# Kernel optimization log

Hardware: AMD Instinct MI355X
Metric: run time of the kernel (lower is better)

The kernel has to match this reference:

```python
import jax, jax.numpy as jnp
import numpy as np

ALPHA = 0.01  # ema_decay

def setup_inputs() -> dict:
    key = jax.random.key(0)
    k1, k2 = jax.random.split(key)
    B, S, H = 8, 2048, 2048
    x = jax.random.normal(k1, (B, S, H), dtype=jnp.float32)
    W = jax.random.normal(k2, (H, H), dtype=jnp.float32) * (1.0 / np.sqrt(H))
    b = jnp.zeros((H,), dtype=jnp.float32)
    return {"x": x, "W": W, "b": b}

def reference(x, W, b):
    B, S, H = x.shape
    dt = x.dtype
    # p = [S-1, S-2, ..., 0]; w_prime = (1-alpha)^p
    p = jnp.arange(S - 1, -1, -1, dtype=dt)
    one_m_a = jnp.asarray(1.0 - ALPHA, dtype=dt)
    w_prime = one_m_a ** p                                   # [S]
    # w = w_prime, but positions t>=1 scaled by alpha
    w = jnp.where(jnp.arange(S) >= 1, w_prime * ALPHA, w_prime)  # [S]
    c = jnp.cumsum(x * w[None, :, None], axis=1)             # [B,S,H]
    s = c / w_prime[None, :, None]                           # [B,S,H]
    # nn.Linear: s @ W^T + b
    return jnp.einsum('bsh,oh->bso', s, W) + b
```

## Files before the change

kernel.cpp:

```cpp
#include <hip/hip_runtime.h>
#include <cstdint>
#include <cstddef>

#define ALPHA 0.01f
#define A1    0.99f
#define B_    8
#define S_    2048
#define H_    2048
#define NCH   8
#define CL    256
#define NKT   32

typedef __attribute__((ext_vector_type(8))) short bf16x8;
typedef __attribute__((ext_vector_type(4))) float f32x4;

__device__ __forceinline__ unsigned short f2bf(float f) {
    unsigned int u = __float_as_uint(f);
    u += 0x7FFFu + ((u >> 16) & 1u);
    return (unsigned short)(u >> 16);
}

__device__ __forceinline__ void gld16(const void* g, void* l) {
    __builtin_amdgcn_global_load_lds(
        (const __attribute__((address_space(1))) unsigned int*)g,
        (__attribute__((address_space(3))) unsigned int*)l, 16, 0, 0);
}

__global__ void ema_cast_w(const float* __restrict__ W, short* __restrict__ Wb) {
    int i = (blockIdx.x * 256 + threadIdx.x) * 4;
    float4 v = *(const float4*)(W + i);
    short4 o;
    o.x = (short)f2bf(v.x);
    o.y = (short)f2bf(v.y);
    o.z = (short)f2bf(v.z);
    o.w = (short)f2bf(v.w);
    *(short4*)(Wb + i) = o;
}

__global__ __launch_bounds__(256) void ema_carry_kernel(
        const float* __restrict__ x, float* __restrict__ carry) {
    int bid = blockIdx.x;
    int hg = bid & 3;
    int c  = (bid >> 2) & 7;
    int b  = bid >> 5;
    int h0 = (hg << 9) + (threadIdx.x << 1);
    const float2* px = (const float2*)(x + ((size_t)(b * S_) + (size_t)c * CL) * H_ + h0);
    const int STR = H_ / 2;
    float s0, s1;
    int i0;
    if (c == 0) { float2 v = px[0]; s0 = v.x; s1 = v.y; i0 = 1; }
    else        { s0 = 0.f; s1 = 0.f;                   i0 = 0; }
    #pragma unroll 8
    for (int i = i0; i < CL; ++i) {
        float2 v = px[(size_t)i * STR];
        s0 = fmaf(A1, s0, ALPHA * v.x);
        s1 = fmaf(A1, s1, ALPHA * v.y);
    }
    *(float2*)(carry + ((b << 3) + c) * H_ + h0) = (float2){s0, s1};
}

__global__ __launch_bounds__(256) void ema_apply_kernel(
        const float* __restrict__ x, const float* __restrict__ carry,
        unsigned short* __restrict__ sb) {
    int bid = blockIdx.x;
    int hg = bid & 3;
    int c  = (bid >> 2) & 7;
    int b  = bid >> 5;
    int h0 = (hg << 9) + (threadIdx.x << 1);

    float A256 = A1;
    #pragma unroll
    for (int q = 0; q < 8; ++q) A256 *= A256;

    float c0 = 0.f, c1 = 0.f, f = 1.f;
    for (int j = c - 1; j >= 0; --j) {
        float2 cv = *(const float2*)(carry + ((b << 3) + j) * H_ + h0);
        c0 = fmaf(cv.x, f, c0);
        c1 = fmaf(cv.y, f, c1);
        f *= A256;
    }

    size_t base = ((size_t)(b * S_) + (size_t)c * CL) * H_ + h0;
    const float2* px = (const float2*)(x + base);
    unsigned int*  pu = (unsigned int*)(sb + base);
    const int STR = H_ / 2;
    float s0, s1;
    int i0;
    if (c == 0) {
        float2 v = px[0]; s0 = v.x; s1 = v.y;
        pu[0] = (unsigned int)f2bf(s0) | ((unsigned int)f2bf(s1) << 16);
        i0 = 1;
    } else { s0 = c0; s1 = c1; i0 = 0; }
    #pragma unroll 8
    for (int i = i0; i < CL; ++i) {
        float2 v = px[(size_t)i * STR];
        s0 = fmaf(A1, s0, ALPHA * v.x);
        s1 = fmaf(A1, s1, ALPHA * v.y);
        pu[(size_t)i * STR] = (unsigned int)f2bf(s0) | ((unsigned int)f2bf(s1) << 16);
    }
}


#define BAR __builtin_amdgcn_s_barrier()
#define VMW(n) asm volatile("s_waitcnt vmcnt(" #n ")" ::: "memory")

#define STGA(i, kt, buf) gld16(gA[i] + (size_t)(kt) * 128, &ldsA[buf][((i) << 12) + (w << 9)])
#define STGB(i, kt, buf) gld16(gB[i] + (size_t)(kt) * 128, &ldsB[buf][((i) << 12) + (w << 9)])

#define LDA(dst, mh) do { int ra_ = (wm << 1) | (mh);                              \
    const char* base_ = (const char*)&ldsA[cur][0]                                 \
        + (((((ra_ & 1) << 1) | (ra_ >> 1))) << 13) + laneRow;                     \
    _Pragma("unroll") for (int m_ = 0; m_ < 4; ++m_) {                             \
        dst[m_][0] = *(const bf16x8*)(base_ + (m_ << 11) + ck0);                   \
        dst[m_][1] = *(const bf16x8*)(base_ + (m_ << 11) + ck1); } } while (0)

#define LDB(nh) do { const char* base_ = (const char*)&ldsB[cur][0]                \
        + ((nh) << 14) + (wn << 12) + laneRow;                                     \
    _Pragma("unroll") for (int n_ = 0; n_ < 2; ++n_) {                             \
        Bf[(nh) * 2 + n_][0] = *(const bf16x8*)(base_ + (n_ << 11) + ck0);         \
        Bf[(nh) * 2 + n_][1] = *(const bf16x8*)(base_ + (n_ << 11) + ck1); } } while (0)

#define MM(Asrc, mh, nh) do { __builtin_amdgcn_s_setprio(1);                       \
    _Pragma("unroll") for (int m_ = 0; m_ < 4; ++m_)                               \
    _Pragma("unroll") for (int n_ = 0; n_ < 2; ++n_)                               \
    _Pragma("unroll") for (int k_ = 0; k_ < 2; ++k_)                               \
        acc[(mh) * 4 + m_][(nh) * 2 + n_] = __builtin_amdgcn_mfma_f32_16x16x32_bf16( \
            Asrc[m_][k_], Bf[(nh) * 2 + n_][k_], acc[(mh) * 4 + m_][(nh) * 2 + n_], 0, 0, 0); \
    __builtin_amdgcn_s_setprio(0); } while (0)

__global__ __launch_bounds__(512, 2) void ema_gemm_kernel(
        const short* __restrict__ Sb, const short* __restrict__ Wb,
        const float* __restrict__ bias, float* __restrict__ out) {
    __shared__ short ldsA[2][16384];
    __shared__ short ldsB[2][16384];

    int bid = blockIdx.x;
    int swz = ((bid & 7) << 6) | (bid >> 3);
    int tm = swz >> 3;
    int tn = swz & 7;

    int tid  = threadIdx.x;
    int lane = tid & 63;
    int w    = tid >> 6;
    int wm   = w >> 2;
    int wn   = w & 3;

    const int K2 = H_ * 2;
    int rowA = tm << 8;
    int rowB = tn << 8;

    int rowoff = (w << 3) + (lane >> 3);
    int colb   = (((lane & 7) ^ (lane >> 3)) << 4);
    const char* SbB = (const char*)Sb;
    const char* WbB = (const char*)Wb;
    const char* gA[4];
    const char* gB[4];
    #pragma unroll
    for (int i = 0; i < 4; ++i) {
        int lq = ((i & 1) << 1) | (i >> 1);
        gA[i] = SbB + (size_t)(rowA + lq * 64 + rowoff) * K2 + colb;
        int pos = 2 * i + (w >> 2);
        int ls  = ((pos & 3) << 1) | (pos >> 2);
        gB[i] = WbB + (size_t)(rowB + ls * 32 + ((w & 3) << 3) + (lane >> 3)) * K2 + colb;
    }

    int laneRow = (lane & 15) << 7;
    int ck0 = (((lane >> 4)) ^ (lane & 7)) << 4;
    int ck1 = ((4 + (lane >> 4)) ^ (lane & 7)) << 4;

    f32x4 acc[8][4];
    #pragma unroll
    for (int i = 0; i < 8; ++i)
        #pragma unroll
        for (int j = 0; j < 4; ++j)
            acc[i][j] = (f32x4){0.f, 0.f, 0.f, 0.f};
    bf16x8 Af0[4][2], Af1[4][2], Bf[4][2];

    int colg = (tn << 8) + (wn << 6) + (lane & 15);
    float bb[4];
    #pragma unroll
    for (int n = 0; n < 4; ++n) bb[n] = bias[colg + (n << 4)];

    STGA(0, 0, 0); STGA(1, 0, 0); STGB(0, 0, 0); STGB(1, 0, 0);
    STGA(2, 0, 0); STGA(3, 0, 0); STGB(2, 0, 0); STGB(3, 0, 0);
    STGA(0, 1, 1); STGA(1, 1, 1); STGB(0, 1, 1); STGB(1, 1, 1);
    VMW(6);
    BAR;

    for (int t = 0; t < NKT; ++t) {
        int cur = t & 1, nxt = cur ^ 1;
        bool i01 = (t < NKT - 1), i23 = (t < NKT - 2);
        LDA(Af0, 0); LDB(0);
        if (i01) { STGA(2, t + 1, nxt); STGA(3, t + 1, nxt); VMW(6); }
        BAR;
        MM(Af0, 0, 0);
        LDB(1);
        if (i01) { STGB(2, t + 1, nxt); STGB(3, t + 1, nxt); }
        BAR;
        MM(Af0, 0, 1);
        LDA(Af1, 1);
        if (i23) { STGA(0, t + 2, cur); STGA(1, t + 2, cur); }
        BAR;
        MM(Af1, 1, 0);
        if (i23)                { STGB(0, t + 2, cur); STGB(1, t + 2, cur); VMW(6); }
        else if (t == NKT - 2)  { VMW(0); }
        BAR;
        MM(Af1, 1, 1);
    }

    int rowg = (tm << 8) + (wm << 7) + ((lane >> 4) << 2);
    #pragma unroll
    for (int m = 0; m < 8; ++m) {
        #pragma unroll
        for (int n = 0; n < 4; ++n) {
            int c = colg + (n << 4);
            size_t rb = (size_t)(rowg + (m << 4)) << 11;
            #pragma unroll
            for (int q = 0; q < 4; ++q)
                out[rb + ((size_t)q << 11) + c] = acc[m][n][q] + bb[n];
        }
    }
}

extern "C" void kernel_launch(void* const* d_in, const int* in_sizes, int n_in,
                              void* d_out, int out_size, void* d_ws, size_t ws_size,
                              hipStream_t stream) {
    const float* x    = (const float*)d_in[0];
    const float* W    = (const float*)d_in[1];
    const float* bias = (const float*)d_in[2];
    float* out = (float*)d_out;

    char* ws = (char*)d_ws;
    size_t s_bytes = (size_t)B_ * S_ * H_ * 2;
    size_t w_bytes = (size_t)H_ * H_ * 2;
    unsigned short* s_bf  = (unsigned short*)ws;
    short*          w_bf  = (short*)(ws + s_bytes);
    float*          carry = (float*)(ws + s_bytes + w_bytes);

    ema_cast_w<<<(H_ * H_) / 1024, 256, 0, stream>>>(W, w_bf);
    ema_carry_kernel<<<B_ * NCH * (H_ / 512), 256, 0, stream>>>(x, carry);
    ema_apply_kernel<<<B_ * NCH * (H_ / 512), 256, 0, stream>>>(x, carry, s_bf);
    ema_gemm_kernel<<<(16384 / 256) * (2048 / 256), 512, 0, stream>>>(
        (const short*)s_bf, w_bf, bias, out);
}
```

Baseline: 186.3 us.

## Use triple-buffered K=32 tiles with one barrier per GEMM iteration

```diff
diff --git a/kernel.cpp b/kernel.cpp
--- a/kernel.cpp
+++ b/kernel.cpp
@@ -9,7 +9,7 @@
 #define H_    2048
 #define NCH   8
 #define CL    256
-#define NKT   32
+#define NKT   64
 
 typedef __attribute__((ext_vector_type(8))) short bf16x8;
 typedef __attribute__((ext_vector_type(4))) float f32x4;
@@ -101,38 +101,38 @@
 }
 
 
-#define BAR __builtin_amdgcn_s_barrier()
+#define BARM asm volatile("s_barrier" ::: "memory")
 #define VMW(n) asm volatile("s_waitcnt vmcnt(" #n ")" ::: "memory")
 
-#define STGA(i, kt, buf) gld16(gA[i] + (size_t)(kt) * 128, &ldsA[buf][((i) << 12) + (w << 9)])
-#define STGB(i, kt, buf) gld16(gB[i] + (size_t)(kt) * 128, &ldsB[buf][((i) << 12) + (w << 9)])
-
-#define LDA(dst, mh) do { int ra_ = (wm << 1) | (mh);                              \
-    const char* base_ = (const char*)&ldsA[cur][0]                                 \
-        + (((((ra_ & 1) << 1) | (ra_ >> 1))) << 13) + laneRow;                     \
-    _Pragma("unroll") for (int m_ = 0; m_ < 4; ++m_) {                             \
-        dst[m_][0] = *(const bf16x8*)(base_ + (m_ << 11) + ck0);                   \
-        dst[m_][1] = *(const bf16x8*)(base_ + (m_ << 11) + ck1); } } while (0)
-
-#define LDB(nh) do { const char* base_ = (const char*)&ldsB[cur][0]                \
-        + ((nh) << 14) + (wn << 12) + laneRow;                                     \
-    _Pragma("unroll") for (int n_ = 0; n_ < 2; ++n_) {                             \
-        Bf[(nh) * 2 + n_][0] = *(const bf16x8*)(base_ + (n_ << 11) + ck0);         \
-        Bf[(nh) * 2 + n_][1] = *(const bf16x8*)(base_ + (n_ << 11) + ck1); } } while (0)
+#define STG(kt, buf) do {                                                          \
+    gld16(gA0 + (size_t)(kt) * 64, &ldsA[buf][(w << 9)]);                          \
+    gld16(gA1 + (size_t)(kt) * 64, &ldsA[buf][4096 + (w << 9)]);                   \
+    gld16(gB0 + (size_t)(kt) * 64, &ldsB[buf][(w << 9)]);                          \
+    gld16(gB1 + (size_t)(kt) * 64, &ldsB[buf][4096 + (w << 9)]); } while (0)
+
+#define LDA(dst, mh) do {                                                          \
+    const char* base_ = (const char*)&ldsA[bc][0] + (wm << 13) + ((mh) << 12)      \
+                        + laneRow + ck;                                            \
+    _Pragma("unroll") for (int m_ = 0; m_ < 4; ++m_)                               \
+        dst[m_] = *(const bf16x8*)(base_ + (m_ << 10)); } while (0)
+
+#define LDB do {                                                                   \
+    const char* base_ = (const char*)&ldsB[bc][0] + (wn << 12) + laneRow + ck;     \
+    _Pragma("unroll") for (int n_ = 0; n_ < 4; ++n_)                               \
+        Bf[n_] = *(const bf16x8*)(base_ + (n_ << 10)); } while (0)
 
 #define MM(Asrc, mh, nh) do { __builtin_amdgcn_s_setprio(1);                       \
     _Pragma("unroll") for (int m_ = 0; m_ < 4; ++m_)                               \
     _Pragma("unroll") for (int n_ = 0; n_ < 2; ++n_)                               \
-    _Pragma("unroll") for (int k_ = 0; k_ < 2; ++k_)                               \
         acc[(mh) * 4 + m_][(nh) * 2 + n_] = __builtin_amdgcn_mfma_f32_16x16x32_bf16( \
-            Asrc[m_][k_], Bf[(nh) * 2 + n_][k_], acc[(mh) * 4 + m_][(nh) * 2 + n_], 0, 0, 0); \
+            Asrc[m_], Bf[(nh) * 2 + n_], acc[(mh) * 4 + m_][(nh) * 2 + n_], 0, 0, 0); \
     __builtin_amdgcn_s_setprio(0); } while (0)
 
 __global__ __launch_bounds__(512, 2) void ema_gemm_kernel(
         const short* __restrict__ Sb, const short* __restrict__ Wb,
         const float* __restrict__ bias, float* __restrict__ out) {
-    __shared__ short ldsA[2][16384];
-    __shared__ short ldsB[2][16384];
+    __shared__ short ldsA[3][8192];
+    __shared__ short ldsB[3][8192];
 
     int bid = blockIdx.x;
     int swz = ((bid & 7) << 6) | (bid >> 3);
@@ -149,24 +149,15 @@
     int rowA = tm << 8;
     int rowB = tn << 8;
 
-    int rowoff = (w << 3) + (lane >> 3);
-    int colb   = (((lane & 7) ^ (lane >> 3)) << 4);
-    const char* SbB = (const char*)Sb;
-    const char* WbB = (const char*)Wb;
-    const char* gA[4];
-    const char* gB[4];
-    #pragma unroll
-    for (int i = 0; i < 4; ++i) {
-        int lq = ((i & 1) << 1) | (i >> 1);
-        gA[i] = SbB + (size_t)(rowA + lq * 64 + rowoff) * K2 + colb;
-        int pos = 2 * i + (w >> 2);
-        int ls  = ((pos & 3) << 1) | (pos >> 2);
-        gB[i] = WbB + (size_t)(rowB + ls * 32 + ((w & 3) << 3) + (lane >> 3)) * K2 + colb;
-    }
-
-    int laneRow = (lane & 15) << 7;
-    int ck0 = (((lane >> 4)) ^ (lane & 7)) << 4;
-    int ck1 = ((4 + (lane >> 4)) ^ (lane & 7)) << 4;
+    int strow = (w << 4) + (lane >> 2);
+    int colb  = (((lane & 3) ^ ((lane >> 2) & 3)) << 4);
+    const char* gA0 = (const char*)Sb + (size_t)(rowA + strow) * K2 + colb;
+    const char* gA1 = (const char*)Sb + (size_t)(rowA + 128 + strow) * K2 + colb;
+    const char* gB0 = (const char*)Wb + (size_t)(rowB + strow) * K2 + colb;
+    const char* gB1 = (const char*)Wb + (size_t)(rowB + 128 + strow) * K2 + colb;
+
+    int laneRow = (lane & 15) << 6;
+    int ck = ((lane >> 4) ^ (lane & 3)) << 4;
 
     f32x4 acc[8][4];
     #pragma unroll
@@ -174,38 +165,31 @@
         #pragma unroll
         for (int j = 0; j < 4; ++j)
             acc[i][j] = (f32x4){0.f, 0.f, 0.f, 0.f};
-    bf16x8 Af0[4][2], Af1[4][2], Bf[4][2];
+    bf16x8 Af0[4], Af1[4], Bf[4];
 
     int colg = (tn << 8) + (wn << 6) + (lane & 15);
     float bb[4];
     #pragma unroll
     for (int n = 0; n < 4; ++n) bb[n] = bias[colg + (n << 4)];
 
-    STGA(0, 0, 0); STGA(1, 0, 0); STGB(0, 0, 0); STGB(1, 0, 0);
-    STGA(2, 0, 0); STGA(3, 0, 0); STGB(2, 0, 0); STGB(3, 0, 0);
-    STGA(0, 1, 1); STGA(1, 1, 1); STGB(0, 1, 1); STGB(1, 1, 1);
-    VMW(6);
-    BAR;
-
+    STG(0, 0);
+    STG(1, 1);
+    VMW(4);
+    BARM;
+
+    int bc = 0, bs = 2;
     for (int t = 0; t < NKT; ++t) {
-        int cur = t & 1, nxt = cur ^ 1;
-        bool i01 = (t < NKT - 1), i23 = (t < NKT - 2);
-        LDA(Af0, 0); LDB(0);
-        if (i01) { STGA(2, t + 1, nxt); STGA(3, t + 1, nxt); VMW(6); }
-        BAR;
+        LDA(Af0, 0); LDB; LDA(Af1, 1);
+        if (t < NKT - 2) { STG(t + 2, bs); }
         MM(Af0, 0, 0);
-        LDB(1);
-        if (i01) { STGB(2, t + 1, nxt); STGB(3, t + 1, nxt); }
-        BAR;
         MM(Af0, 0, 1);
-        LDA(Af1, 1);
-        if (i23) { STGA(0, t + 2, cur); STGA(1, t + 2, cur); }
-        BAR;
         MM(Af1, 1, 0);
-        if (i23)                { STGB(0, t + 2, cur); STGB(1, t + 2, cur); VMW(6); }
-        else if (t == NKT - 2)  { VMW(0); }
-        BAR;
         MM(Af1, 1, 1);
+        if (t < NKT - 2)       { VMW(4); }
+        else if (t == NKT - 2) { VMW(0); }
+        BARM;
+        bc = (bc == 2) ? 0 : bc + 1;
+        bs = (bs == 2) ? 0 : bs + 1;
     }
 
     int rowg = (tm << 8) + (wm << 7) + ((lane >> 4) << 2);
```

Measured after the change: 204.1 us. +9.6%, slower.
